# Kernel tuning notes

Measured on AMD Instinct MI355X. Metric: run time of the kernel, lower is better.

## Reference

```python
import jax, jax.numpy as jnp
import numpy as np

N_RES = 4096
N_PAIRS = 500000

def setup_inputs() -> dict:
    key = jax.random.key(0)
    k1, k2, k3 = jax.random.split(key, 3)
    ca_coords = jax.random.normal(k1, (N_RES, 3), dtype=jnp.float32) * 10.0
    K = jax.random.uniform(k2, (N_RES, N_RES), dtype=jnp.float32)
    pairs = jax.random.randint(k3, (N_PAIRS, 2), 0, N_RES, dtype=jnp.int64)
    return {"ca_coords": ca_coords, "K": K, "pairs": pairs}


def _reconstruct_backbone(ca):
    # vectorized version of reconstruct_backbone_atoms
    n = ca.shape[0]
    vec = ca[1:] - ca[:-1]                                  # (n-1,3)
    unit = vec / (jnp.linalg.norm(vec, axis=-1, keepdims=True) + 1e-8)
    # N atoms: n_coords[i] = ca[i] - 0.38*unit(ca[i]-ca[i-1]); n_coords[0] uses unit[0]
    n_coords = jnp.concatenate([ca[:1] - 0.38 * unit[:1], ca[1:] - 0.38 * unit], axis=0)
    # C atoms: c_coords[i] = ca[i] + 0.38*unit(ca[i+1]-ca[i]); c_coords[-1] uses unit[-1]
    c_coords = jnp.concatenate([ca[:-1] + 0.38 * unit, ca[-1:] + 0.38 * unit[-1:]], axis=0)
    # O atoms: perpendicular to (C-CA, N-CA) plane, last residue special-cased
    vec_n = n_coords[:-1] - ca[:-1]
    vec_c = c_coords[:-1] - ca[:-1]
    perp = jnp.cross(vec_c, vec_n)
    pnorm = jnp.linalg.norm(perp, axis=-1, keepdims=True)
    perp = jnp.where(pnorm > 1e-6, perp / jnp.maximum(pnorm, 1e-12), perp)
    o_body = c_coords[:-1] + 1.24 * perp
    o_last = c_coords[-1:] + jnp.array([[0.0, 1.24, 0.0]], dtype=ca.dtype)
    o_coords = jnp.concatenate([o_body, o_last], axis=0)
    return n_coords, c_coords, o_coords


def _pairwise_dist(x, y):
    # safe cdist: sqrt clamped so diagonal zeros stay differentiable
    sq = jnp.sum((x[:, None, :] - y[None, :, :]) ** 2, axis=-1)
    return jnp.sqrt(jnp.maximum(sq, 1e-12))


def reference(ca_coords, K, pairs):
    n = ca_coords.shape[0]

    # --- bond energy (weight=30): mean((|ca[i+1]-ca[i]| - 3.8)^2) ---
    d_bond = jnp.linalg.norm(ca_coords[1:] - ca_coords[:-1], axis=-1)
    e_bond = 30.0 * jnp.mean((d_bond - 3.8) ** 2)

    # --- clash energy (weight=50): mean(relu(3.2 - d_pair)^2) ---
    dv = ca_coords[pairs[:, 0]] - ca_coords[pairs[:, 1]]
    d_pair = jnp.sqrt(jnp.maximum(jnp.sum(dv ** 2, axis=-1), 1e-12))
    e_clash = 50.0 * jnp.mean(jax.nn.relu(3.2 - d_pair) ** 2)

    # --- contact energy (weight=5): mean((D - 8*(1-K))^2) over full NxN ---
    D = _pairwise_dist(ca_coords, ca_coords)
    target = 8.0 * (1.0 - K)
    e_contact = 5.0 * jnp.mean((D - target) ** 2)

    # --- hydrogen bond energy (weight=4) from reconstructed backbone ---
    n_coords, c_coords, o_coords = _reconstruct_backbone(ca_coords)
    ideal = 2.95
    hb = jnp.float32(0.0)
    # double loop i, j in [i+2, i+6) -> offsets 2..5, vectorized per offset
    for off in (2, 3, 4, 5):
        d = jnp.linalg.norm(o_coords[: n - off] - n_coords[off:], axis=-1)
        pen = jnp.exp(-(((d - ideal) / 0.3) ** 2))
        hb = hb - 0.5 * jnp.sum(jnp.where((d > 2.5) & (d < 3.5), pen, 0.0))
    e_hb = 4.0 * hb / (n * n)

    return e_bond + e_clash + e_contact + e_hb
```

## Files before the change

kernel.cpp:

```cpp
#include <hip/hip_runtime.h>
#include <math.h>

#define NRES   4096
#define NBLK   512
#define ROWS   8
#define NQ     (NRES / 4)
#define CHUNKS (NQ / 256)

__device__ __forceinline__ float wave_sum(float v) {
#pragma unroll
    for (int off = 32; off > 0; off >>= 1) v += __shfl_down(v, off, 64);
    return v;
}

__global__ __launch_bounds__(256) void energy_kernel(const float* __restrict__ ca,
                                                     const float* __restrict__ K,
                                                     const int* __restrict__ pairs,
                                                     float4* __restrict__ partial,
                                                     int npairs) {
    __shared__ float sx[NRES], sy[NRES], sz[NRES];
    __shared__ float red[4][4];
    const int tid = threadIdx.x;
    const int b   = blockIdx.x;

    for (int j = tid; j < NRES; j += 256) {
        sx[j] = ca[3*j+0];
        sy[j] = ca[3*j+1];
        sz[j] = ca[3*j+2];
    }
    __syncthreads();

    const int row0 = b * ROWS;
    float xi[ROWS], yi[ROWS], zi[ROWS];
#pragma unroll
    for (int r = 0; r < ROWS; ++r) {
        xi[r] = sx[row0 + r]; yi[r] = sy[row0 + r]; zi[r] = sz[row0 + r];
    }

    float contact = 0.f;
    const float4* Kp = (const float4*)(K + (size_t)row0 * NRES);
#pragma unroll
    for (int k = 0; k < CHUNKS; ++k) {
        const int j4 = tid + (k << 8);
        float4 kv[ROWS];
#pragma unroll
        for (int r = 0; r < ROWS; ++r) kv[r] = Kp[(size_t)r * NQ + j4];
        const int j = j4 << 2;
        const float4 cx = *(const float4*)&sx[j];
        const float4 cy = *(const float4*)&sy[j];
        const float4 cz = *(const float4*)&sz[j];
#pragma unroll
        for (int r = 0; r < ROWS; ++r) {
            float dx, dy, dz, sq, D, t;
            dx = xi[r]-cx.x; dy = yi[r]-cy.x; dz = zi[r]-cz.x;
            sq = fmaf(dx, dx, fmaf(dy, dy, dz*dz));
            D  = sqrtf(fmaxf(sq, 1e-12f));
            t  = fmaf(8.f, kv[r].x, D - 8.f);
            contact = fmaf(t, t, contact);

            dx = xi[r]-cx.y; dy = yi[r]-cy.y; dz = zi[r]-cz.y;
            sq = fmaf(dx, dx, fmaf(dy, dy, dz*dz));
            D  = sqrtf(fmaxf(sq, 1e-12f));
            t  = fmaf(8.f, kv[r].y, D - 8.f);
            contact = fmaf(t, t, contact);

            dx = xi[r]-cx.z; dy = yi[r]-cy.z; dz = zi[r]-cz.z;
            sq = fmaf(dx, dx, fmaf(dy, dy, dz*dz));
            D  = sqrtf(fmaxf(sq, 1e-12f));
            t  = fmaf(8.f, kv[r].z, D - 8.f);
            contact = fmaf(t, t, contact);

            dx = xi[r]-cx.w; dy = yi[r]-cy.w; dz = zi[r]-cz.w;
            sq = fmaf(dx, dx, fmaf(dy, dy, dz*dz));
            D  = sqrtf(fmaxf(sq, 1e-12f));
            t  = fmaf(8.f, kv[r].w, D - 8.f);
            contact = fmaf(t, t, contact);
        }
    }

    float clash = 0.f;
    for (int p = b * 256 + tid; p < npairs; p += NBLK * 256) {
        int2 pr = ((const int2*)pairs)[p];
        float dx = sx[pr.x] - sx[pr.y];
        float dy = sy[pr.x] - sy[pr.y];
        float dz = sz[pr.x] - sz[pr.y];
        float d  = sqrtf(fmaxf(fmaf(dx, dx, fmaf(dy, dy, dz*dz)), 1e-12f));
        float r  = fmaxf(3.2f - d, 0.f);
        clash = fmaf(r, r, clash);
    }

    float bond = 0.f, hb = 0.f;
    if (tid < ROWS) {
        const int i = row0 + tid;
        const int n = NRES;

        if (i < n - 1) {
            float dx = sx[i+1]-sx[i], dy = sy[i+1]-sy[i], dz = sz[i+1]-sz[i];
            float d  = sqrtf(fmaf(dx, dx, fmaf(dy, dy, dz*dz)));
            float t  = d - 3.8f;
            bond = t * t;
        }

        if (i < n - 2) {
            float cax = sx[i], cay = sy[i], caz = sz[i];
            float vx = sx[i+1]-cax, vy = sy[i+1]-cay, vz = sz[i+1]-caz;
            float inv = 1.f / (sqrtf(vx*vx + vy*vy + vz*vz) + 1e-8f);
            float ux = vx*inv, uy = vy*inv, uz = vz*inv;

            float upx, upy, upz;
            if (i == 0) { upx = ux; upy = uy; upz = uz; }
            else {
                float wx = cax-sx[i-1], wy = cay-sy[i-1], wz = caz-sz[i-1];
                float inv2 = 1.f / (sqrtf(wx*wx + wy*wy + wz*wz) + 1e-8f);
                upx = wx*inv2; upy = wy*inv2; upz = wz*inv2;
            }

            float vcx = 0.38f*ux,  vcy = 0.38f*uy,  vcz = 0.38f*uz;
            float vnx = -0.38f*upx, vny = -0.38f*upy, vnz = -0.38f*upz;
            float px = vcy*vnz - vcz*vny;
            float py = vcz*vnx - vcx*vnz;
            float pz = vcx*vny - vcy*vnx;
            float pn = sqrtf(px*px + py*py + pz*pz);
            if (pn > 1e-6f) {
                float ipn = 1.f / fmaxf(pn, 1e-12f);
                px *= ipn; py *= ipn; pz *= ipn;
            }
            float ox = cax + vcx + 1.24f*px;
            float oy = cay + vcy + 1.24f*py;
            float oz = caz + vcz + 1.24f*pz;

#pragma unroll
            for (int off = 2; off <= 5; ++off) {
                int jj = i + off;
                if (jj < n) {
                    float cjx = sx[jj], cjy = sy[jj], cjz = sz[jj];
                    float qx = cjx-sx[jj-1], qy = cjy-sy[jj-1], qz = cjz-sz[jj-1];
                    float invq = 1.f / (sqrtf(qx*qx + qy*qy + qz*qz) + 1e-8f);
                    float njx = cjx - 0.38f*qx*invq;
                    float njy = cjy - 0.38f*qy*invq;
                    float njz = cjz - 0.38f*qz*invq;
                    float ddx = ox-njx, ddy = oy-njy, ddz = oz-njz;
                    float d = sqrtf(ddx*ddx + ddy*ddy + ddz*ddz);
                    if (d > 2.5f && d < 3.5f) {
                        float z = (d - 2.95f) * (1.0f / 0.3f);
                        hb -= 0.5f * expf(-z*z);
                    }
                }
            }
        }
    }

    float vb = wave_sum(bond);
    float vc = wave_sum(clash);
    float vk = wave_sum(contact);
    float vh = wave_sum(hb);
    const int wave = tid >> 6;
    if ((tid & 63) == 0) {
        red[wave][0] = vb; red[wave][1] = vc; red[wave][2] = vk; red[wave][3] = vh;
    }
    __syncthreads();
    if (tid == 0) {
        float4 out;
        out.x = red[0][0] + red[1][0] + red[2][0] + red[3][0];
        out.y = red[0][1] + red[1][1] + red[2][1] + red[3][1];
        out.z = red[0][2] + red[1][2] + red[2][2] + red[3][2];
        out.w = red[0][3] + red[1][3] + red[2][3] + red[3][3];
        partial[b] = out;
    }
}

__global__ __launch_bounds__(256) void finalize_kernel(const float4* __restrict__ partial,
                                                       float* __restrict__ out,
                                                       int n, int npairs) {
    __shared__ float red[4][4];
    const int tid = threadIdx.x;
    float4 a = partial[tid];
    float4 c = partial[tid + 256];
    float vb = a.x + c.x, vc = a.y + c.y, vk = a.z + c.z, vh = a.w + c.w;
    vb = wave_sum(vb); vc = wave_sum(vc); vk = wave_sum(vk); vh = wave_sum(vh);
    const int wave = tid >> 6;
    if ((tid & 63) == 0) {
        red[wave][0] = vb; red[wave][1] = vc; red[wave][2] = vk; red[wave][3] = vh;
    }
    __syncthreads();
    if (tid == 0) {
        float bond    = red[0][0] + red[1][0] + red[2][0] + red[3][0];
        float clash   = red[0][1] + red[1][1] + red[2][1] + red[3][1];
        float contact = red[0][2] + red[1][2] + red[2][2] + red[3][2];
        float hb      = red[0][3] + red[1][3] + red[2][3] + red[3][3];
        float inv_nn  = 1.f / ((float)n * (float)n);
        float e = 30.f * bond / (float)(n - 1)
                + 50.f * clash / (float)npairs
                + 5.f  * contact * inv_nn
                + 4.f  * hb * inv_nn;
        out[0] = e;
    }
}

extern "C" void kernel_launch(void* const* d_in, const int* in_sizes, int n_in,
                              void* d_out, int out_size, void* d_ws, size_t ws_size,
                              hipStream_t stream) {
    const float* ca    = (const float*)d_in[0];
    const float* K     = (const float*)d_in[1];
    const int*   pairs = (const int*)d_in[2];
    float* out = (float*)d_out;
    float4* partial = (float4*)d_ws;

    int n      = in_sizes[0] / 3;
    int npairs = in_sizes[2] / 2;

    energy_kernel<<<NBLK, 256, 0, stream>>>(ca, K, pairs, partial, npairs);
    finalize_kernel<<<1, 256, 0, stream>>>(partial, out, n, npairs);
}
```

Baseline: 111.1 us.

## Split contact tiles into column halves, software-pipeline K loads, move side terms to global

```diff
diff --git a/kernel.cpp b/kernel.cpp
--- a/kernel.cpp
+++ b/kernel.cpp
@@ -1,11 +1,11 @@
 #include <hip/hip_runtime.h>
 #include <math.h>
 
-#define NRES   4096
-#define NBLK   512
-#define ROWS   8
-#define NQ     (NRES / 4)
-#define CHUNKS (NQ / 256)
+#define NRES 4096
+#define ROWS 8
+#define COLS 2048
+#define NBLK ((NRES / ROWS) * (NRES / COLS))
+#define HB_BLOCKS (NRES / 256)
 
 __device__ __forceinline__ float wave_sum(float v) {
 #pragma unroll
@@ -13,104 +13,133 @@
     return v;
 }
 
-__global__ __launch_bounds__(256) void energy_kernel(const float* __restrict__ ca,
-                                                     const float* __restrict__ K,
-                                                     const int* __restrict__ pairs,
-                                                     float4* __restrict__ partial,
-                                                     int npairs) {
-    __shared__ float sx[NRES], sy[NRES], sz[NRES];
+__device__ __forceinline__ float c4(float4 kv, float4 cx, float4 cy, float4 cz,
+                                    float xi, float yi, float zi, float s) {
+    float dx, dy, dz, sq, D, t;
+    dx = xi - cx.x; dy = yi - cy.x; dz = zi - cz.x;
+    sq = fmaf(dx, dx, fmaf(dy, dy, dz * dz));
+    D  = sqrtf(sq);
+    t  = fmaf(8.f, kv.x, D - 8.f);
+    s  = fmaf(t, t, s);
+
+    dx = xi - cx.y; dy = yi - cy.y; dz = zi - cz.y;
+    sq = fmaf(dx, dx, fmaf(dy, dy, dz * dz));
+    D  = sqrtf(sq);
+    t  = fmaf(8.f, kv.y, D - 8.f);
+    s  = fmaf(t, t, s);
+
+    dx = xi - cx.z; dy = yi - cy.z; dz = zi - cz.z;
+    sq = fmaf(dx, dx, fmaf(dy, dy, dz * dz));
+    D  = sqrtf(sq);
+    t  = fmaf(8.f, kv.z, D - 8.f);
+    s  = fmaf(t, t, s);
+
+    dx = xi - cx.w; dy = yi - cy.w; dz = zi - cz.w;
+    sq = fmaf(dx, dx, fmaf(dy, dy, dz * dz));
+    D  = sqrtf(sq);
+    t  = fmaf(8.f, kv.w, D - 8.f);
+    s  = fmaf(t, t, s);
+    return s;
+}
+
+__global__ __launch_bounds__(256, 4) void energy_kernel(const float* __restrict__ ca,
+                                                        const float* __restrict__ K,
+                                                        const int* __restrict__ pairs,
+                                                        float4* __restrict__ partial,
+                                                        int npairs) {
+    __shared__ float sx[COLS], sy[COLS], sz[COLS];
     __shared__ float red[4][4];
-    const int tid = threadIdx.x;
-    const int b   = blockIdx.x;
-
-    for (int j = tid; j < NRES; j += 256) {
-        sx[j] = ca[3*j+0];
-        sy[j] = ca[3*j+1];
-        sz[j] = ca[3*j+2];
+    const int tid  = threadIdx.x;
+    const int b    = blockIdx.x;
+    const int tile = b & 1;
+    const int row0 = (b >> 1) * ROWS;
+    const int c0   = tile * COLS;
+
+    for (int j = tid; j < COLS; j += 256) {
+        int g = c0 + j;
+        sx[j] = ca[3 * g + 0];
+        sy[j] = ca[3 * g + 1];
+        sz[j] = ca[3 * g + 2];
     }
     __syncthreads();
 
-    const int row0 = b * ROWS;
     float xi[ROWS], yi[ROWS], zi[ROWS];
 #pragma unroll
     for (int r = 0; r < ROWS; ++r) {
-        xi[r] = sx[row0 + r]; yi[r] = sy[row0 + r]; zi[r] = sz[row0 + r];
-    }
-
+        int g = row0 + r;
+        xi[r] = ca[3 * g + 0];
+        yi[r] = ca[3 * g + 1];
+        zi[r] = ca[3 * g + 2];
+    }
+
+    const float* Kb = K + (size_t)row0 * NRES + c0;
+    const int j0 = tid << 2;
+    const int j1 = (tid + 256) << 2;
     float contact = 0.f;
-    const float4* Kp = (const float4*)(K + (size_t)row0 * NRES);
-#pragma unroll
-    for (int k = 0; k < CHUNKS; ++k) {
-        const int j4 = tid + (k << 8);
-        float4 kv[ROWS];
-#pragma unroll
-        for (int r = 0; r < ROWS; ++r) kv[r] = Kp[(size_t)r * NQ + j4];
-        const int j = j4 << 2;
-        const float4 cx = *(const float4*)&sx[j];
-        const float4 cy = *(const float4*)&sy[j];
-        const float4 cz = *(const float4*)&sz[j];
-#pragma unroll
-        for (int r = 0; r < ROWS; ++r) {
-            float dx, dy, dz, sq, D, t;
-            dx = xi[r]-cx.x; dy = yi[r]-cy.x; dz = zi[r]-cz.x;
-            sq = fmaf(dx, dx, fmaf(dy, dy, dz*dz));
-            D  = sqrtf(fmaxf(sq, 1e-12f));
-            t  = fmaf(8.f, kv[r].x, D - 8.f);
-            contact = fmaf(t, t, contact);
-
-            dx = xi[r]-cx.y; dy = yi[r]-cy.y; dz = zi[r]-cz.y;
-            sq = fmaf(dx, dx, fmaf(dy, dy, dz*dz));
-            D  = sqrtf(fmaxf(sq, 1e-12f));
-            t  = fmaf(8.f, kv[r].y, D - 8.f);
-            contact = fmaf(t, t, contact);
-
-            dx = xi[r]-cx.z; dy = yi[r]-cy.z; dz = zi[r]-cz.z;
-            sq = fmaf(dx, dx, fmaf(dy, dy, dz*dz));
-            D  = sqrtf(fmaxf(sq, 1e-12f));
-            t  = fmaf(8.f, kv[r].z, D - 8.f);
-            contact = fmaf(t, t, contact);
-
-            dx = xi[r]-cx.w; dy = yi[r]-cy.w; dz = zi[r]-cz.w;
-            sq = fmaf(dx, dx, fmaf(dy, dy, dz*dz));
-            D  = sqrtf(fmaxf(sq, 1e-12f));
-            t  = fmaf(8.f, kv[r].w, D - 8.f);
-            contact = fmaf(t, t, contact);
-        }
-    }
+
+    float4 va[4], vb[4];
+#pragma unroll
+    for (int r = 0; r < 4; ++r) va[r] = *(const float4*)(Kb + (size_t)r * NRES + j0);
+#pragma unroll
+    for (int r = 0; r < 4; ++r) vb[r] = *(const float4*)(Kb + (size_t)(4 + r) * NRES + j0);
+
+    float4 cx0 = *(const float4*)&sx[j0];
+    float4 cy0 = *(const float4*)&sy[j0];
+    float4 cz0 = *(const float4*)&sz[j0];
+
+#pragma unroll
+    for (int r = 0; r < 4; ++r) contact = c4(va[r], cx0, cy0, cz0, xi[r], yi[r], zi[r], contact);
+#pragma unroll
+    for (int r = 0; r < 4; ++r) va[r] = *(const float4*)(Kb + (size_t)r * NRES + j1);
+#pragma unroll
+    for (int r = 0; r < 4; ++r) contact = c4(vb[r], cx0, cy0, cz0, xi[4 + r], yi[4 + r], zi[4 + r], contact);
+#pragma unroll
+    for (int r = 0; r < 4; ++r) vb[r] = *(const float4*)(Kb + (size_t)(4 + r) * NRES + j1);
+
+    float4 cx1 = *(const float4*)&sx[j1];
+    float4 cy1 = *(const float4*)&sy[j1];
+    float4 cz1 = *(const float4*)&sz[j1];
+
+#pragma unroll
+    for (int r = 0; r < 4; ++r) contact = c4(va[r], cx1, cy1, cz1, xi[r], yi[r], zi[r], contact);
+#pragma unroll
+    for (int r = 0; r < 4; ++r) contact = c4(vb[r], cx1, cy1, cz1, xi[4 + r], yi[4 + r], zi[4 + r], contact);
 
     float clash = 0.f;
     for (int p = b * 256 + tid; p < npairs; p += NBLK * 256) {
         int2 pr = ((const int2*)pairs)[p];
-        float dx = sx[pr.x] - sx[pr.y];
-        float dy = sy[pr.x] - sy[pr.y];
-        float dz = sz[pr.x] - sz[pr.y];
-        float d  = sqrtf(fmaxf(fmaf(dx, dx, fmaf(dy, dy, dz*dz)), 1e-12f));
+        float dx = ca[3 * pr.x + 0] - ca[3 * pr.y + 0];
+        float dy = ca[3 * pr.x + 1] - ca[3 * pr.y + 1];
+        float dz = ca[3 * pr.x + 2] - ca[3 * pr.y + 2];
+        float d  = sqrtf(fmaxf(fmaf(dx, dx, fmaf(dy, dy, dz * dz)), 1e-12f));
         float r  = fmaxf(3.2f - d, 0.f);
         clash = fmaf(r, r, clash);
     }
 
     float bond = 0.f, hb = 0.f;
-    if (tid < ROWS) {
-        const int i = row0 + tid;
+    if (b < HB_BLOCKS) {
+        const int i = b * 256 + tid;
         const int n = NRES;
 
         if (i < n - 1) {
-            float dx = sx[i+1]-sx[i], dy = sy[i+1]-sy[i], dz = sz[i+1]-sz[i];
-            float d  = sqrtf(fmaf(dx, dx, fmaf(dy, dy, dz*dz)));
+            float dx = ca[3*(i+1)+0] - ca[3*i+0];
+            float dy = ca[3*(i+1)+1] - ca[3*i+1];
+            float dz = ca[3*(i+1)+2] - ca[3*i+2];
+            float d  = sqrtf(fmaf(dx, dx, fmaf(dy, dy, dz * dz)));
             float t  = d - 3.8f;
             bond = t * t;
         }
 
         if (i < n - 2) {
-            float cax = sx[i], cay = sy[i], caz = sz[i];
-            float vx = sx[i+1]-cax, vy = sy[i+1]-cay, vz = sz[i+1]-caz;
+            float cax = ca[3*i+0], cay = ca[3*i+1], caz = ca[3*i+2];
+            float vx = ca[3*(i+1)+0] - cax, vy = ca[3*(i+1)+1] - cay, vz = ca[3*(i+1)+2] - caz;
             float inv = 1.f / (sqrtf(vx*vx + vy*vy + vz*vz) + 1e-8f);
             float ux = vx*inv, uy = vy*inv, uz = vz*inv;
 
             float upx, upy, upz;
             if (i == 0) { upx = ux; upy = uy; upz = uz; }
             else {
-                float wx = cax-sx[i-1], wy = cay-sy[i-1], wz = caz-sz[i-1];
+                float wx = cax - ca[3*(i-1)+0], wy = cay - ca[3*(i-1)+1], wz = caz - ca[3*(i-1)+2];
                 float inv2 = 1.f / (sqrtf(wx*wx + wy*wy + wz*wz) + 1e-8f);
                 upx = wx*inv2; upy = wy*inv2; upz = wz*inv2;
             }
@@ -133,8 +162,8 @@
             for (int off = 2; off <= 5; ++off) {
                 int jj = i + off;
                 if (jj < n) {
-                    float cjx = sx[jj], cjy = sy[jj], cjz = sz[jj];
-                    float qx = cjx-sx[jj-1], qy = cjy-sy[jj-1], qz = cjz-sz[jj-1];
+                    float cjx = ca[3*jj+0], cjy = ca[3*jj+1], cjz = ca[3*jj+2];
+                    float qx = cjx - ca[3*(jj-1)+0], qy = cjy - ca[3*(jj-1)+1], qz = cjz - ca[3*(jj-1)+2];
                     float invq = 1.f / (sqrtf(qx*qx + qy*qy + qz*qz) + 1e-8f);
                     float njx = cjx - 0.38f*qx*invq;
                     float njy = cjy - 0.38f*qy*invq;
@@ -150,22 +179,22 @@
         }
     }
 
-    float vb = wave_sum(bond);
-    float vc = wave_sum(clash);
-    float vk = wave_sum(contact);
-    float vh = wave_sum(hb);
+    float vbo = wave_sum(bond);
+    float vcl = wave_sum(clash);
+    float vco = wave_sum(contact);
+    float vhb = wave_sum(hb);
     const int wave = tid >> 6;
     if ((tid & 63) == 0) {
-        red[wave][0] = vb; red[wave][1] = vc; red[wave][2] = vk; red[wave][3] = vh;
+        red[wave][0] = vbo; red[wave][1] = vcl; red[wave][2] = vco; red[wave][3] = vhb;
     }
     __syncthreads();
     if (tid == 0) {
-        float4 out;
-        out.x = red[0][0] + red[1][0] + red[2][0] + red[3][0];
-        out.y = red[0][1] + red[1][1] + red[2][1] + red[3][1];
-        out.z = red[0][2] + red[1][2] + red[2][2] + red[3][2];
-        out.w = red[0][3] + red[1][3] + red[2][3] + red[3][3];
-        partial[b] = out;
+        float4 o;
+        o.x = red[0][0] + red[1][0] + red[2][0] + red[3][0];
+        o.y = red[0][1] + red[1][1] + red[2][1] + red[3][1];
+        o.z = red[0][2] + red[1][2] + red[2][2] + red[3][2];
+        o.w = red[0][3] + red[1][3] + red[2][3] + red[3][3];
+        partial[b] = o;
     }
 }
 
@@ -174,9 +203,12 @@
                                                        int n, int npairs) {
     __shared__ float red[4][4];
     const int tid = threadIdx.x;
-    float4 a = partial[tid];
-    float4 c = partial[tid + 256];
-    float vb = a.x + c.x, vc = a.y + c.y, vk = a.z + c.z, vh = a.w + c.w;
+    float vb = 0.f, vc = 0.f, vk = 0.f, vh = 0.f;
+#pragma unroll
+    for (int s = 0; s < NBLK; s += 256) {
+        float4 a = partial[tid + s];
+        vb += a.x; vc += a.y; vk += a.z; vh += a.w;
+    }
     vb = wave_sum(vb); vc = wave_sum(vc); vk = wave_sum(vk); vh = wave_sum(vh);
     const int wave = tid >> 6;
     if ((tid & 63) == 0) {
@@ -189,11 +221,10 @@
         float contact = red[0][2] + red[1][2] + red[2][2] + red[3][2];
         float hb      = red[0][3] + red[1][3] + red[2][3] + red[3][3];
         float inv_nn  = 1.f / ((float)n * (float)n);
-        float e = 30.f * bond / (float)(n - 1)
-                + 50.f * clash / (float)npairs
-                + 5.f  * contact * inv_nn
-                + 4.f  * hb * inv_nn;
-        out[0] = e;
+        out[0] = 30.f * bond / (float)(n - 1)
+               + 50.f * clash / (float)npairs
+               + 5.f  * contact * inv_nn
+               + 4.f  * hb * inv_nn;
     }
 }
 
```

New measurement: 109.0 us. Within noise of the previous version (-1.9%).
